# Kernel tuning notes

Measured on AMD Instinct MI355X. Metric: run time of the kernel, lower is better.

The kernel has to match this reference:

```python
import jax, jax.numpy as jnp
import numpy as np

DIM = 2048
NUM_HEADS = 8
HEAD_DIM = DIM // NUM_HEADS  # 256; forward requires seq_len == HEAD_DIM
B = 64
N = HEAD_DIM  # q @ k (untransposed) only works when N == head_dim


def setup_inputs() -> dict:
    key = jax.random.key(0)
    k1, k2, k3, k4 = jax.random.split(key, 4)
    x = jax.random.normal(k1, (B, N, DIM), dtype=jnp.float32)
    # torch Linear stores weight as [out_features, in_features]
    w_qkv = jax.random.normal(k2, (3 * DIM, DIM), dtype=jnp.float32) * 0.02
    w_proj = jax.random.normal(k3, (DIM, DIM), dtype=jnp.float32) * 0.02
    b_proj = jax.random.normal(k4, (DIM,), dtype=jnp.float32) * 0.02
    return {"x": x, "w_qkv": w_qkv, "w_proj": w_proj, "b_proj": b_proj}


def reference(x, w_qkv, w_proj, b_proj):
    Bb, Nn, C = x.shape
    H, D = NUM_HEADS, C // NUM_HEADS
    # qkv projection (no bias), split into q,k,v of shape [B,H,N,D]
    qkv = (x @ w_qkv.T).reshape(Bb, Nn, 3, H, D).transpose(2, 0, 3, 1, 4)
    q, k, v = qkv[0], qkv[1], qkv[2]
    # NON-standard: q @ k with k NOT transposed -> contracts q's feature dim
    # against k's token dim (valid because D == N). attn: [B,H,N,N]
    attn = jnp.matmul(q, k)
    # transpose last two dims, then softmax over the new last axis
    attn = jnp.swapaxes(attn, -2, -1)
    attn = jax.nn.softmax(attn, axis=-1)
    out = jnp.matmul(attn, v)              # [B,H,N,D]
    out = out.swapaxes(1, 2).reshape(Bb, Nn, C)
    return out @ w_proj.T + b_proj
```

## Files before the change

kernel.cpp:

```cpp
#include <hip/hip_runtime.h>
#include <hip/hip_bf16.h>

typedef unsigned short u16;
typedef __attribute__((ext_vector_type(4))) float f32x4;
typedef __attribute__((ext_vector_type(8))) short short8;
typedef __attribute__((ext_vector_type(8))) u16 us8;


__device__ __forceinline__ u16 f2bf(float f) {
  union { float f; unsigned u; } v; v.f = f;
  unsigned r = v.u + 0x7fffu + ((v.u >> 16) & 1u);
  return (u16)(r >> 16);
}
__device__ __forceinline__ float bf2f(u16 h) {
  union { unsigned u; float f; } v; v.u = ((unsigned)h) << 16; return v.f;
}

__global__ void beacon_kernel(float* __restrict__ out, float val, int n) {
  int stride = gridDim.x * blockDim.x;
  for (int i = blockIdx.x * blockDim.x + threadIdx.x; i < n; i += stride)
    out[i] = val;
}

__global__ void split_kernel(const float* __restrict__ in, u16* __restrict__ hi,
                             u16* __restrict__ lo, int n4) {
  int stride = gridDim.x * blockDim.x;
  for (int i = blockIdx.x * blockDim.x + threadIdx.x; i < n4; i += stride) {
    f32x4 v = ((const f32x4*)in)[i];
    ushort4 h;
    h.x = f2bf(v[0]); h.y = f2bf(v[1]); h.z = f2bf(v[2]); h.w = f2bf(v[3]);
    ((ushort4*)hi)[i] = h;
    if (lo) {
      ushort4 l;
      l.x = f2bf(v[0] - bf2f(h.x)); l.y = f2bf(v[1] - bf2f(h.y));
      l.z = f2bf(v[2] - bf2f(h.z)); l.w = f2bf(v[3] - bf2f(h.w));
      ((ushort4*)lo)[i] = l;
    }
  }
}

#define SCHED0 __builtin_amdgcn_sched_barrier(0)
#define LGKM0 do { asm volatile("s_waitcnt lgkmcnt(0)" ::: "memory"); SCHED0; } while (0)
#define VM0 do { asm volatile("s_waitcnt vmcnt(0)" ::: "memory"); } while (0)
#define BAR __builtin_amdgcn_s_barrier()

template<int EPI>
__global__ __launch_bounds__(512, 2)
void gemm256(const u16* __restrict__ A0, const u16* __restrict__ A1,
             const u16* __restrict__ B0, const u16* __restrict__ B1,
             int ldA, int ldB, int ntiles, int segShift, int gridMx,
             u16* __restrict__ qh, u16* __restrict__ ql,
             u16* __restrict__ kh, u16* __restrict__ kl,
             u16* __restrict__ vv,
             float* __restrict__ fout, const float* __restrict__ bias) {
  extern __shared__ __align__(16) u16 lds[];

  const int tid = threadIdx.x;
  const int w = tid >> 6, lane = tid & 63;
  const int wr = w >> 2, wcn = w & 3;
  const int l15 = lane & 15, g = lane >> 4;
  const int rsw = l15 & 7;
  const int scol = (((tid & 7) ^ ((tid >> 3) & 7)) << 3);

  int bid = blockIdx.x, cpx = gridDim.x >> 3;
  int swz = (bid & 7) * cpx + (bid >> 3);
  int m0 = (swz % gridMx) << 8;
  int n0 = (swz / gridMx) << 8;

  const u16* As[2] = {A0, A1};
  const u16* Bs[2] = {B0, B1};
  const int kmask = (1 << segShift) - 1;

  f32x4 acc[8][4] = {};
  short8 af[8], bA[4], bB[4];

  auto stageA = [&](int db, const u16* Ab, int k0) {
    #pragma unroll
    for (int s = 0; s < 4; ++s) {
      const u16* src = Ab + (size_t)(m0 + s * 64 + (tid >> 3)) * ldA + k0 + scol;
      u16* dst = lds + db * 32768 + s * 4096 + tid * 8;
      __builtin_amdgcn_global_load_lds(
          (const __attribute__((address_space(1))) unsigned*)src,
          (__attribute__((address_space(3))) unsigned*)dst, 16, 0, 0);
    }
  };
  auto stageB = [&](int db, const u16* Bb, int k0) {
    #pragma unroll
    for (int s = 0; s < 4; ++s) {
      const u16* src = Bb + (size_t)(n0 + s * 64 + (tid >> 3)) * ldB + k0 + scol;
      u16* dst = lds + db * 32768 + 16384 + s * 4096 + tid * 8;
      __builtin_amdgcn_global_load_lds(
          (const __attribute__((address_space(1))) unsigned*)src,
          (__attribute__((address_space(3))) unsigned*)dst, 16, 0, 0);
    }
  };
  auto readA = [&](int db, int MH) {
    #pragma unroll
    for (int f = 0; f < 4; ++f) {
      int row = wr * 128 + MH * 64 + f * 16 + l15;
      #pragma unroll
      for (int kk = 0; kk < 2; ++kk) {
        int sl = (kk * 4 + g) ^ rsw;
        af[f * 2 + kk] = *(const short8*)(lds + db * 32768 + row * 64 + sl * 8);
      }
    }
  };
  auto readB = [&](short8* bf, int db, int NH) {
    #pragma unroll
    for (int f = 0; f < 2; ++f) {
      int row = wcn * 64 + NH * 32 + f * 16 + l15;
      #pragma unroll
      for (int kk = 0; kk < 2; ++kk) {
        int sl = (kk * 4 + g) ^ rsw;
        bf[f * 2 + kk] = *(const short8*)(lds + db * 32768 + 16384 + row * 64 + sl * 8);
      }
    }
  };

#define MMA_QUAD(MH, NH, BF)                                                   \
  __builtin_amdgcn_s_setprio(1);                                               \
  _Pragma("unroll") for (int f = 0; f < 4; ++f)                                \
    _Pragma("unroll") for (int j = 0; j < 2; ++j)                              \
      _Pragma("unroll") for (int kk = 0; kk < 2; ++kk)                         \
        acc[(MH) * 4 + f][(NH) * 2 + j] =                                      \
            __builtin_amdgcn_mfma_f32_16x16x32_bf16(                           \
                af[f * 2 + kk], BF[j * 2 + kk],                                \
                acc[(MH) * 4 + f][(NH) * 2 + j], 0, 0, 0);                     \
  __builtin_amdgcn_s_setprio(0)

  const int T = ntiles;
  stageA(0, As[0], 0);
  stageB(0, Bs[0], 0);
  VM0;
  BAR; SCHED0;

  for (int t = 0; t < T - 1; ++t) {
    int cur = t & 1, nxt = cur ^ 1;
    int t1 = t + 1;
    const u16* An = As[t1 >> segShift];
    const u16* Bn = Bs[t1 >> segShift];
    int kn = (t1 & kmask) << 6;
    readA(cur, 0);
    readB(bA, cur, 0);
    stageA(nxt, An, kn);
    BAR; LGKM0;
    MMA_QUAD(0, 0, bA);
    BAR; SCHED0;
    readB(bB, cur, 1);
    stageB(nxt, Bn, kn);
    BAR; LGKM0;
    MMA_QUAD(0, 1, bB);
    BAR; SCHED0;
    readA(cur, 1);
    BAR; LGKM0;
    MMA_QUAD(1, 1, bB);
    BAR; SCHED0;
    MMA_QUAD(1, 0, bA);
    VM0;
    BAR; SCHED0;
  }
  {
    int cur = (T - 1) & 1;
    readA(cur, 0);
    readB(bA, cur, 0);
    LGKM0;
    MMA_QUAD(0, 0, bA);
    readB(bB, cur, 1);
    LGKM0;
    MMA_QUAD(0, 1, bB);
    readA(cur, 1);
    LGKM0;
    MMA_QUAD(1, 1, bB);
    MMA_QUAD(1, 0, bA);
  }
#undef MMA_QUAD

  #pragma unroll
  for (int i = 0; i < 8; ++i)
    #pragma unroll
    for (int j = 0; j < 4; ++j)
      #pragma unroll
      for (int rr = 0; rr < 4; ++rr) {
        int gm = m0 + wr * 128 + i * 16 + g * 4 + rr;
        int gn = n0 + wcn * 64 + j * 16 + l15;
        float val = acc[i][j][rr];
        if constexpr (EPI == 0) {
          int b = gm >> 8, tok = gm & 255;
          int sel = gn >> 11, head = (gn >> 8) & 7, col = gn & 255;
          size_t addr = (((size_t)b * 8 + head) * 256 + tok) * 256 + col;
          u16 h = f2bf(val), lo = f2bf(val - bf2f(h));
          if (sel == 0) { qh[addr] = h; ql[addr] = lo; }
          else          { kh[addr] = h; kl[addr] = lo; }
        } else if constexpr (EPI == 1) {
          int b = gm >> 8, tok = gm & 255;
          int head = (gn >> 8) & 7, col = gn & 255;
          size_t addr = (((size_t)b * 8 + head) * 256 + tok) * 256 + col;
          vv[addr] = f2bf(val);
        } else {
          fout[(size_t)gm * 2048 + gn] = val + bias[gn];
        }
      }
}

__global__ __launch_bounds__(256)
void attn_fused(const u16* __restrict__ kh, const u16* __restrict__ kl,
                const u16* __restrict__ qh, const u16* __restrict__ ql,
                u16* __restrict__ P) {
  __shared__ __align__(16) u16 sA[4096];
  __shared__ __align__(16) u16 sB[8192];
  const int tid = threadIdx.x;
  const int wave = tid >> 6, lane = tid & 63;
  const int l15 = lane & 15, l16 = lane >> 4;
  const int sxor = (l15 >> 1) & 3;
  const int scol = ((lane & 3) ^ ((lane >> 3) & 3)) * 8;
  const int m0 = blockIdx.x << 7;
  const size_t zo = (size_t)blockIdx.y * 65536;
  const u16* As[3] = {kh + zo, kh + zo, kl + zo};
  const u16* Bs[3] = {qh + zo, ql + zo, qh + zo};

  f32x4 acc[2][16] = {};

  for (int ks = 0; ks < 24; ++ks) {
    int seg = ks >> 3, k0 = (ks & 7) * 32;
    {
      const u16* gp = As[seg];
      #pragma unroll
      for (int c = 0; c < 2; ++c) {
        int chunk = wave + c * 4;
        int r = chunk * 16 + (lane >> 2);
        const u16* src = gp + (size_t)(m0 + r) * 256 + k0 + scol;
        __builtin_amdgcn_global_load_lds(
            (const __attribute__((address_space(1))) unsigned*)src,
            (__attribute__((address_space(3))) unsigned*)(sA + chunk * 512), 16, 0, 0);
      }
    }
    {
      const u16* gp = Bs[seg];
      #pragma unroll
      for (int c = 0; c < 4; ++c) {
        int chunk = wave + c * 4;
        int r = chunk * 16 + (lane >> 2);
        const u16* src = gp + (size_t)r * 256 + k0 + scol;
        __builtin_amdgcn_global_load_lds(
            (const __attribute__((address_space(1))) unsigned*)src,
            (__attribute__((address_space(3))) unsigned*)(sB + chunk * 512), 16, 0, 0);
      }
    }
    __syncthreads();

    short8 a[2];
    #pragma unroll
    for (int i = 0; i < 2; ++i) {
      int ra = (wave * 32 + i * 16 + l15) * 4 + (l16 ^ sxor);
      a[i] = ((const short8*)sA)[ra];
    }
    #pragma unroll
    for (int h = 0; h < 2; ++h) {
      short8 b[8];
      #pragma unroll
      for (int c = 0; c < 8; ++c) {
        int rb = ((h * 8 + c) * 16 + l15) * 4 + (l16 ^ sxor);
        b[c] = ((const short8*)sB)[rb];
      }
      #pragma unroll
      for (int i = 0; i < 2; ++i)
        #pragma unroll
        for (int c = 0; c < 8; ++c)
          acc[i][h * 8 + c] = __builtin_amdgcn_mfma_f32_16x16x32_bf16(
              a[i], b[c], acc[i][h * 8 + c], 0, 0, 0);
    }
    __syncthreads();
  }

  u16* Pp = P + zo;
  #pragma unroll
  for (int i = 0; i < 2; ++i)
    #pragma unroll
    for (int rr = 0; rr < 4; ++rr) {
      float m = acc[i][0][rr];
      #pragma unroll
      for (int c = 1; c < 16; ++c) m = fmaxf(m, acc[i][c][rr]);
      #pragma unroll
      for (int sh = 1; sh < 16; sh <<= 1) m = fmaxf(m, __shfl_xor(m, sh));
      float e[16];
      float s = 0.f;
      #pragma unroll
      for (int c = 0; c < 16; ++c) { e[c] = __expf(acc[i][c][rr] - m); s += e[c]; }
      #pragma unroll
      for (int sh = 1; sh < 16; sh <<= 1) s += __shfl_xor(s, sh);
      float inv = 1.0f / s;
      int row = m0 + wave * 32 + i * 16 + l16 * 4 + rr;
      #pragma unroll
      for (int c = 0; c < 16; ++c)
        Pp[(size_t)row * 256 + c * 16 + l15] = f2bf(e[c] * inv);
    }
}

template<int EPI>
__global__ __launch_bounds__(256)
void gemm_nt(const u16* __restrict__ A0, const u16* __restrict__ B0,
             u16* __restrict__ aout, int ksteps) {
  __shared__ __align__(16) u16 lds[8192];
  u16* sA = lds;
  u16* sB = lds + 4096;

  const int tid = threadIdx.x;
  const int wave = tid >> 6, lane = tid & 63;
  const int wr = wave >> 1, wc = wave & 1;
  const int l15 = lane & 15, l16 = lane >> 4;
  const int sxor = (l15 >> 1) & 3;

  size_t zoff = (size_t)blockIdx.z * 65536;
  const u16* Ab = A0 + zoff;
  const u16* Bb = B0 + zoff;

  const int m0 = blockIdx.x << 7;
  const int n0 = blockIdx.y << 7;

  f32x4 acc[4][4] = {};

  auto stage = [&](const u16* gp, u16* slot, int row0, int k0) {
    int scol = ((lane & 3) ^ ((lane >> 3) & 3)) * 8;
    #pragma unroll
    for (int c = 0; c < 2; ++c) {
      int chunk = wave + c * 4;
      int r = chunk * 16 + (lane >> 2);
      const u16* src = gp + (size_t)(row0 + r) * 256 + (k0 + scol);
      __builtin_amdgcn_global_load_lds(
          (const __attribute__((address_space(1))) unsigned*)src,
          (__attribute__((address_space(3))) unsigned*)(slot + chunk * 512), 16, 0, 0);
    }
  };

  for (int ks = 0; ks < ksteps; ++ks) {
    int k0 = ks * 32;
    stage(Ab, sA, m0, k0);
    stage(Bb, sB, n0, k0);
    __syncthreads();

    short8 a[4], b[4];
    #pragma unroll
    for (int i = 0; i < 4; ++i) {
      int ra = (wr * 64 + i * 16 + l15) * 4 + (l16 ^ sxor);
      int rb = (wc * 64 + i * 16 + l15) * 4 + (l16 ^ sxor);
      a[i] = ((const short8*)sA)[ra];
      b[i] = ((const short8*)sB)[rb];
    }
    #pragma unroll
    for (int i = 0; i < 4; ++i)
      #pragma unroll
      for (int j = 0; j < 4; ++j)
        acc[i][j] = __builtin_amdgcn_mfma_f32_16x16x32_bf16(a[i], b[j], acc[i][j], 0, 0, 0);
    __syncthreads();
  }

  #pragma unroll
  for (int i = 0; i < 4; ++i)
    #pragma unroll
    for (int j = 0; j < 4; ++j)
      #pragma unroll
      for (int r = 0; r < 4; ++r) {
        int gm = m0 + wr * 64 + i * 16 + l16 * 4 + r;
        int gn = n0 + wc * 64 + j * 16 + l15;
        int gp = blockIdx.z;
        size_t row = (size_t)(gp >> 3) * 256 + gm;
        size_t col = (size_t)(gp & 7) * 256 + gn;
        aout[row * 2048 + col] = f2bf(acc[i][j][r]);
      }
}

__global__ void transpose_inplace(u16* __restrict__ kh, u16* __restrict__ kl,
                                  u16* __restrict__ v) {
  __shared__ u16 ta[64][66], tb[64][66];
  u16* base = (blockIdx.z == 0) ? kh : (blockIdx.z == 1) ? kl : v;
  u16* pl = base + (size_t)blockIdx.y * 65536;
  const int RA[10] = {0,1,2,3, 0,0,0,1,1,2};
  const int CA[10] = {0,1,2,3, 1,2,3,2,3,3};
  int p = blockIdx.x;
  int R = RA[p], C = CA[p];
  bool diag = (R == C);
  int tid = threadIdx.x;
  int r = tid >> 2, c0 = (tid & 3) * 16;

  const us8* sa = (const us8*)(pl + (size_t)(R * 64 + r) * 256 + C * 64 + c0);
  us8 a0 = sa[0], a1 = sa[1];
  #pragma unroll
  for (int s = 0; s < 8; ++s) { ta[r][c0 + s] = a0[s]; ta[r][c0 + 8 + s] = a1[s]; }
  if (!diag) {
    const us8* sb = (const us8*)(pl + (size_t)(C * 64 + r) * 256 + R * 64 + c0);
    us8 b0 = sb[0], b1 = sb[1];
    #pragma unroll
    for (int s = 0; s < 8; ++s) { tb[r][c0 + s] = b0[s]; tb[r][c0 + 8 + s] = b1[s]; }
  }
  __syncthreads();
  us8 o0, o1;
  #pragma unroll
  for (int s = 0; s < 8; ++s) { o0[s] = ta[c0 + s][r]; o1[s] = ta[c0 + 8 + s][r]; }
  us8* da = (us8*)(pl + (size_t)(C * 64 + r) * 256 + R * 64 + c0);
  da[0] = o0; da[1] = o1;
  if (!diag) {
    us8 p0, p1;
    #pragma unroll
    for (int s = 0; s < 8; ++s) { p0[s] = tb[c0 + s][r]; p1[s] = tb[c0 + 8 + s][r]; }
    us8* db = (us8*)(pl + (size_t)(R * 64 + r) * 256 + C * 64 + c0);
    db[0] = p0; db[1] = p1;
  }
}

extern "C" void kernel_launch(void* const* d_in, const int* in_sizes, int n_in,
                              void* d_out, int out_size, void* d_ws, size_t ws_size,
                              hipStream_t stream) {
  const float* x  = (const float*)d_in[0];
  const float* wq = (const float*)d_in[1];
  const float* wp = (const float*)d_in[2];
  const float* bp = (const float*)d_in[3];
  float* out = (float*)d_out;
  char* ws = (char*)d_ws;

  const size_t MB = 1ull << 20;
  const size_t NEED = 432 * MB;
  if (ws_size < NEED) {
    beacon_kernel<<<2048, 256, 0, stream>>>(out, (float)(ws_size >> 20), 16384 * 2048);
    return;
  }

  u16* q_hi = (u16*)(ws);
  u16* q_lo = (u16*)(ws + 64 * MB);
  u16* k_hi = (u16*)(ws + 128 * MB);
  u16* k_lo = (u16*)(ws + 192 * MB);
  u16* vbuf = (u16*)(ws + 256 * MB);
  u16* x_hi = (u16*)(ws + 320 * MB);
  u16* w_hi = (u16*)(ws + 384 * MB);
  u16* w_lo = (u16*)(ws + 408 * MB);
  u16* Pm   = (u16*)(ws + 320 * MB);
  u16* attn = (u16*)(ws + 128 * MB);
  u16* wpb  = (u16*)(ws + 384 * MB);

  split_kernel<<<8192, 256, 0, stream>>>(x,  x_hi, nullptr, 16384 * 2048 / 4);
  split_kernel<<<4096, 256, 0, stream>>>(wq, w_hi, w_lo, 6144 * 2048 / 4);

  gemm256<0><<<1024, 512, 131072, stream>>>(
      x_hi, x_hi, w_hi, w_lo, 2048, 2048, 64, 5, 64,
      q_hi, q_lo, k_hi, k_lo, nullptr, nullptr, nullptr);
  const u16* wv = w_hi + (size_t)4096 * 2048;
  gemm256<1><<<512, 512, 131072, stream>>>(
      x_hi, x_hi, wv, wv, 2048, 2048, 32, 5, 64,
      nullptr, nullptr, nullptr, nullptr, vbuf, nullptr, nullptr);

  transpose_inplace<<<dim3(10, 512, 3), 256, 0, stream>>>(k_hi, k_lo, vbuf);

  attn_fused<<<dim3(2, 512), 256, 0, stream>>>(k_hi, k_lo, q_hi, q_lo, Pm);

  gemm_nt<3><<<dim3(2, 2, 512), 256, 0, stream>>>(Pm, vbuf, attn, 8);

  split_kernel<<<2048, 256, 0, stream>>>(wp, wpb, nullptr, 2048 * 2048 / 4);
  gemm256<2><<<512, 512, 131072, stream>>>(
      attn, attn, wpb, wpb, 2048, 2048, 32, 5, 64,
      nullptr, nullptr, nullptr, nullptr, nullptr, out, bp);
}
```

Before: 1.093 ms.

## Fuse softmax-probability GEMM with P@V, keeping P in shared memory

Merges the score+softmax kernel and the separate P@V GEMM into one kernel. The normalized probabilities are written to a padded LDS tile rather than to global memory, then multiplied against V staged from global. The row tile per block shrinks from 128 to 64, so the grid doubles. This removes the global write and re-read of the P matrix and one kernel launch. In exchange it uses more LDS per block, which may lower occupancy, and each block re-streams all of V.

```diff
diff --git a/kernel.cpp b/kernel.cpp
--- a/kernel.cpp
+++ b/kernel.cpp
@@ -203,36 +203,34 @@
 }
 
 __global__ __launch_bounds__(256)
-void attn_fused(const u16* __restrict__ kh, const u16* __restrict__ kl,
+void fused_attn(const u16* __restrict__ kh, const u16* __restrict__ kl,
                 const u16* __restrict__ qh, const u16* __restrict__ ql,
-                u16* __restrict__ P) {
-  __shared__ __align__(16) u16 sA[4096];
+                const u16* __restrict__ vT, u16* __restrict__ aout) {
+  __shared__ __align__(16) u16 sA[2048];
   __shared__ __align__(16) u16 sB[8192];
+  __shared__ __align__(16) u16 sP[64 * 276];
+
   const int tid = threadIdx.x;
   const int wave = tid >> 6, lane = tid & 63;
   const int l15 = lane & 15, l16 = lane >> 4;
   const int sxor = (l15 >> 1) & 3;
   const int scol = ((lane & 3) ^ ((lane >> 3) & 3)) * 8;
-  const int m0 = blockIdx.x << 7;
+  const int m0 = blockIdx.x << 6;
   const size_t zo = (size_t)blockIdx.y * 65536;
   const u16* As[3] = {kh + zo, kh + zo, kl + zo};
   const u16* Bs[3] = {qh + zo, ql + zo, qh + zo};
 
-  f32x4 acc[2][16] = {};
-
+  f32x4 acc[16] = {};
   for (int ks = 0; ks < 24; ++ks) {
     int seg = ks >> 3, k0 = (ks & 7) * 32;
     {
       const u16* gp = As[seg];
-      #pragma unroll
-      for (int c = 0; c < 2; ++c) {
-        int chunk = wave + c * 4;
-        int r = chunk * 16 + (lane >> 2);
-        const u16* src = gp + (size_t)(m0 + r) * 256 + k0 + scol;
-        __builtin_amdgcn_global_load_lds(
-            (const __attribute__((address_space(1))) unsigned*)src,
-            (__attribute__((address_space(3))) unsigned*)(sA + chunk * 512), 16, 0, 0);
-      }
+      int chunk = wave;
+      int r = chunk * 16 + (lane >> 2);
+      const u16* src = gp + (size_t)(m0 + r) * 256 + k0 + scol;
+      __builtin_amdgcn_global_load_lds(
+          (const __attribute__((address_space(1))) unsigned*)src,
+          (__attribute__((address_space(3))) unsigned*)(sA + chunk * 512), 16, 0, 0);
     }
     {
       const u16* gp = Bs[seg];
@@ -248,124 +246,89 @@
     }
     __syncthreads();
 
-    short8 a[2];
+    short8 a;
+    {
+      int ra = (wave * 16 + l15) * 4 + (l16 ^ sxor);
+      a = ((const short8*)sA)[ra];
+    }
+    #pragma unroll
+    for (int c = 0; c < 16; ++c) {
+      int rb = (c * 16 + l15) * 4 + (l16 ^ sxor);
+      short8 b = ((const short8*)sB)[rb];
+      acc[c] = __builtin_amdgcn_mfma_f32_16x16x32_bf16(a, b, acc[c], 0, 0, 0);
+    }
+    __syncthreads();
+  }
+
+  #pragma unroll
+  for (int rr = 0; rr < 4; ++rr) {
+    float m = acc[0][rr];
+    #pragma unroll
+    for (int c = 1; c < 16; ++c) m = fmaxf(m, acc[c][rr]);
+    #pragma unroll
+    for (int sh = 1; sh < 16; sh <<= 1) m = fmaxf(m, __shfl_xor(m, sh));
+    float e[16];
+    float s = 0.f;
+    #pragma unroll
+    for (int c = 0; c < 16; ++c) { e[c] = __expf(acc[c][rr] - m); s += e[c]; }
+    #pragma unroll
+    for (int sh = 1; sh < 16; sh <<= 1) s += __shfl_xor(s, sh);
+    float inv = 1.0f / s;
+    int prow = wave * 16 + l16 * 4 + rr;
+    #pragma unroll
+    for (int c = 0; c < 16; ++c)
+      sP[prow * 276 + c * 16 + l15] = f2bf(e[c] * inv);
+  }
+  __syncthreads();
+
+  const int wr2 = wave >> 1, wc2 = wave & 1;
+  f32x4 acc2[2][8] = {};
+  for (int ks = 0; ks < 8; ++ks) {
+    int k0 = ks * 32;
+    {
+      #pragma unroll
+      for (int c = 0; c < 4; ++c) {
+        int chunk = wave + c * 4;
+        int r = chunk * 16 + (lane >> 2);
+        const u16* src = vT + zo + (size_t)r * 256 + k0 + scol;
+        __builtin_amdgcn_global_load_lds(
+            (const __attribute__((address_space(1))) unsigned*)src,
+            (__attribute__((address_space(3))) unsigned*)(sB + chunk * 512), 16, 0, 0);
+      }
+    }
+    __syncthreads();
+
+    short8 a[2], b[8];
     #pragma unroll
     for (int i = 0; i < 2; ++i) {
-      int ra = (wave * 32 + i * 16 + l15) * 4 + (l16 ^ sxor);
-      a[i] = ((const short8*)sA)[ra];
-    }
-    #pragma unroll
-    for (int h = 0; h < 2; ++h) {
-      short8 b[8];
-      #pragma unroll
-      for (int c = 0; c < 8; ++c) {
-        int rb = ((h * 8 + c) * 16 + l15) * 4 + (l16 ^ sxor);
-        b[c] = ((const short8*)sB)[rb];
-      }
-      #pragma unroll
-      for (int i = 0; i < 2; ++i)
-        #pragma unroll
-        for (int c = 0; c < 8; ++c)
-          acc[i][h * 8 + c] = __builtin_amdgcn_mfma_f32_16x16x32_bf16(
-              a[i], b[c], acc[i][h * 8 + c], 0, 0, 0);
-    }
+      int prow = wr2 * 32 + i * 16 + l15;
+      a[i] = *(const short8*)(sP + prow * 276 + k0 + l16 * 8);
+    }
+    #pragma unroll
+    for (int j = 0; j < 8; ++j) {
+      int rb = ((wc2 * 128 + j * 16 + l15)) * 4 + (l16 ^ sxor);
+      b[j] = ((const short8*)sB)[rb];
+    }
+    #pragma unroll
+    for (int i = 0; i < 2; ++i)
+      #pragma unroll
+      for (int j = 0; j < 8; ++j)
+        acc2[i][j] = __builtin_amdgcn_mfma_f32_16x16x32_bf16(a[i], b[j], acc2[i][j], 0, 0, 0);
     __syncthreads();
   }
 
-  u16* Pp = P + zo;
+  int plane = blockIdx.y;
   #pragma unroll
   for (int i = 0; i < 2; ++i)
     #pragma unroll
-    for (int rr = 0; rr < 4; ++rr) {
-      float m = acc[i][0][rr];
-      #pragma unroll
-      for (int c = 1; c < 16; ++c) m = fmaxf(m, acc[i][c][rr]);
-      #pragma unroll
-      for (int sh = 1; sh < 16; sh <<= 1) m = fmaxf(m, __shfl_xor(m, sh));
-      float e[16];
-      float s = 0.f;
-      #pragma unroll
-      for (int c = 0; c < 16; ++c) { e[c] = __expf(acc[i][c][rr] - m); s += e[c]; }
-      #pragma unroll
-      for (int sh = 1; sh < 16; sh <<= 1) s += __shfl_xor(s, sh);
-      float inv = 1.0f / s;
-      int row = m0 + wave * 32 + i * 16 + l16 * 4 + rr;
-      #pragma unroll
-      for (int c = 0; c < 16; ++c)
-        Pp[(size_t)row * 256 + c * 16 + l15] = f2bf(e[c] * inv);
-    }
-}
-
-template<int EPI>
-__global__ __launch_bounds__(256)
-void gemm_nt(const u16* __restrict__ A0, const u16* __restrict__ B0,
-             u16* __restrict__ aout, int ksteps) {
-  __shared__ __align__(16) u16 lds[8192];
-  u16* sA = lds;
-  u16* sB = lds + 4096;
-
-  const int tid = threadIdx.x;
-  const int wave = tid >> 6, lane = tid & 63;
-  const int wr = wave >> 1, wc = wave & 1;
-  const int l15 = lane & 15, l16 = lane >> 4;
-  const int sxor = (l15 >> 1) & 3;
-
-  size_t zoff = (size_t)blockIdx.z * 65536;
-  const u16* Ab = A0 + zoff;
-  const u16* Bb = B0 + zoff;
-
-  const int m0 = blockIdx.x << 7;
-  const int n0 = blockIdx.y << 7;
-
-  f32x4 acc[4][4] = {};
-
-  auto stage = [&](const u16* gp, u16* slot, int row0, int k0) {
-    int scol = ((lane & 3) ^ ((lane >> 3) & 3)) * 8;
-    #pragma unroll
-    for (int c = 0; c < 2; ++c) {
-      int chunk = wave + c * 4;
-      int r = chunk * 16 + (lane >> 2);
-      const u16* src = gp + (size_t)(row0 + r) * 256 + (k0 + scol);
-      __builtin_amdgcn_global_load_lds(
-          (const __attribute__((address_space(1))) unsigned*)src,
-          (__attribute__((address_space(3))) unsigned*)(slot + chunk * 512), 16, 0, 0);
-    }
-  };
-
-  for (int ks = 0; ks < ksteps; ++ks) {
-    int k0 = ks * 32;
-    stage(Ab, sA, m0, k0);
-    stage(Bb, sB, n0, k0);
-    __syncthreads();
-
-    short8 a[4], b[4];
-    #pragma unroll
-    for (int i = 0; i < 4; ++i) {
-      int ra = (wr * 64 + i * 16 + l15) * 4 + (l16 ^ sxor);
-      int rb = (wc * 64 + i * 16 + l15) * 4 + (l16 ^ sxor);
-      a[i] = ((const short8*)sA)[ra];
-      b[i] = ((const short8*)sB)[rb];
-    }
-    #pragma unroll
-    for (int i = 0; i < 4; ++i)
-      #pragma unroll
-      for (int j = 0; j < 4; ++j)
-        acc[i][j] = __builtin_amdgcn_mfma_f32_16x16x32_bf16(a[i], b[j], acc[i][j], 0, 0, 0);
-    __syncthreads();
-  }
-
-  #pragma unroll
-  for (int i = 0; i < 4; ++i)
-    #pragma unroll
-    for (int j = 0; j < 4; ++j)
-      #pragma unroll
-      for (int r = 0; r < 4; ++r) {
-        int gm = m0 + wr * 64 + i * 16 + l16 * 4 + r;
-        int gn = n0 + wc * 64 + j * 16 + l15;
-        int gp = blockIdx.z;
-        size_t row = (size_t)(gp >> 3) * 256 + gm;
-        size_t col = (size_t)(gp & 7) * 256 + gn;
-        aout[row * 2048 + col] = f2bf(acc[i][j][r]);
+    for (int j = 0; j < 8; ++j)
+      #pragma unroll
+      for (int rr = 0; rr < 4; ++rr) {
+        int gi = m0 + wr2 * 32 + i * 16 + l16 * 4 + rr;
+        int gd = wc2 * 128 + j * 16 + l15;
+        size_t row = (size_t)(plane >> 3) * 256 + gi;
+        size_t col = (size_t)(plane & 7) * 256 + gd;
+        aout[row * 2048 + col] = f2bf(acc2[i][j][rr]);
       }
 }
 
@@ -432,8 +395,7 @@
   u16* x_hi = (u16*)(ws + 320 * MB);
   u16* w_hi = (u16*)(ws + 384 * MB);
   u16* w_lo = (u16*)(ws + 408 * MB);
-  u16* Pm   = (u16*)(ws + 320 * MB);
-  u16* attn = (u16*)(ws + 128 * MB);
+  u16* attn = (u16*)(ws + 320 * MB);
   u16* wpb  = (u16*)(ws + 384 * MB);
 
   split_kernel<<<8192, 256, 0, stream>>>(x,  x_hi, nullptr, 16384 * 2048 / 4);
@@ -449,9 +411,7 @@
 
   transpose_inplace<<<dim3(10, 512, 3), 256, 0, stream>>>(k_hi, k_lo, vbuf);
 
-  attn_fused<<<dim3(2, 512), 256, 0, stream>>>(k_hi, k_lo, q_hi, q_lo, Pm);
-
-  gemm_nt<3><<<dim3(2, 2, 512), 256, 0, stream>>>(Pm, vbuf, attn, 8);
+  fused_attn<<<dim3(4, 512), 256, 0, stream>>>(k_hi, k_lo, q_hi, q_lo, vbuf, attn);
 
   split_kernel<<<2048, 256, 0, stream>>>(wp, wpb, nullptr, 2048 * 2048 / 4);
   gemm256<2><<<512, 512, 131072, stream>>>(
```

Measured after the change: 1.072 ms. Within noise of the previous version (-1.9%).
